# Performance work log

Hardware: AMD Instinct MI355X
Metric: run time of the kernel (lower is better)

Reference implementation:

```python
import jax, jax.numpy as jnp
import numpy as np

MARGIN = 0.5          # TripletLoss(margin=0.5)
N_FEAT = 100000       # gallery size N (rows of `features`)
D = 128               # embedding dim
N_BATCH = 256         # batch size n
N_CLASSES = 1000      # number of identities -> ~100 positives per class


def setup_inputs() -> dict:
    key = jax.random.key(0)
    k1, k2 = jax.random.split(key)
    inputs = jax.random.normal(k1, (N_BATCH, D), dtype=jnp.float32)
    features = jax.random.normal(k2, (N_FEAT, D), dtype=jnp.float32)
    # feature_labels encodes the t2i dict: label of every gallery row.
    feature_labels = (jnp.arange(N_FEAT, dtype=jnp.int32) % N_CLASSES).astype(jnp.int32)
    # idx[i] is the gallery row corresponding to batch sample i (distinct rows).
    idx = jnp.arange(N_BATCH, dtype=jnp.int32)
    # consistency: targets[i] must equal feature_labels[idx[i]]
    targets = feature_labels[idx]
    return {"inputs": inputs, "features": features, "targets": targets,
            "feature_labels": feature_labels, "idx": idx}


def reference(inputs, features, targets, feature_labels, idx):
    # sim_mat = inputs @ features.T  -> [n, N]
    sim = jnp.matmul(inputs, features.T)
    n_feat = features.shape[0]
    # pos: same identity, excluding the sample's own gallery row idx[i]
    same = feature_labels[None, :] == targets[:, None]          # [n, N]
    is_self = jnp.arange(n_feat, dtype=idx.dtype)[None, :] == idx[:, None]
    pos_mask = same & ~is_self
    neg_mask = ~same
    big = jnp.asarray(jnp.finfo(sim.dtype).max, sim.dtype)
    pos = jnp.min(jnp.where(pos_mask, sim, big), axis=1)        # hardest positive (min sim)
    neg = jnp.max(jnp.where(neg_mask, sim, -big), axis=1)       # hardest negative (max sim)
    loss = jax.nn.relu(neg - pos + MARGIN)                      # [n]
    return jnp.sum(loss) / targets.shape[0]
```

## Files before the change

### kernel.cpp

```cpp
#include <hip/hip_runtime.h>

#define NFEAT   100000
#define NBATCH  256
#define DIM     128
#define MARGIN_F 0.5f
#define FLT_BIG 3.402823466e+38f

#define GRID    250
#define CHUNKS  25
#define CROWS   16
#define RPB     (CHUNKS * CROWS)
#define CBYTES  (CROWS * DIM * 2)

#define GRIDF   1250
#define RPBF    80
#define NTILEF  5

typedef __bf16 bf8_t  __attribute__((ext_vector_type(8)));
typedef short  sh8_t  __attribute__((ext_vector_type(8)));
typedef float  f32x4  __attribute__((ext_vector_type(4)));

__device__ __forceinline__ bf8_t pack8(float4 v0, float4 v1) {
  bf8_t r;
  r[0] = (__bf16)v0.x; r[1] = (__bf16)v0.y; r[2] = (__bf16)v0.z; r[3] = (__bf16)v0.w;
  r[4] = (__bf16)v1.x; r[5] = (__bf16)v1.y; r[6] = (__bf16)v1.z; r[7] = (__bf16)v1.w;
  return r;
}

template <typename VA, typename VC>
__device__ __forceinline__ auto mfma_sel(VA a, VA b, VC c, int)
    -> decltype(__builtin_amdgcn_mfma_f32_16x16x32_bf16(a, b, c, 0, 0, 0)) {
  return __builtin_amdgcn_mfma_f32_16x16x32_bf16(a, b, c, 0, 0, 0);
}
template <typename VA, typename VC>
__device__ __forceinline__ VC mfma_sel(VA a, VA b, VC c, long) {
  return __builtin_amdgcn_mfma_f32_16x16x32_bf16(
      __builtin_bit_cast(sh8_t, a), __builtin_bit_cast(sh8_t, b), c, 0, 0, 0);
}
__device__ __forceinline__ f32x4 mfma_bf16(bf8_t a, bf8_t b, f32x4 c) {
  return mfma_sel(a, b, c, 0);
}

#if defined(__has_builtin)
#if __has_builtin(__builtin_amdgcn_global_load_lds)
#define HAVE_GLLDS 1
#endif
#endif

__device__ __forceinline__ void stage16(const char* g, char* l) {
#ifdef HAVE_GLLDS
  __builtin_amdgcn_global_load_lds(
      (const __attribute__((address_space(1))) unsigned int*)g,
      (__attribute__((address_space(3))) unsigned int*)l, 16, 0, 0);
#else
  *reinterpret_cast<float4*>(l) = *reinterpret_cast<const float4*>(g);
#endif
}

#define CFENCE()  asm volatile("" ::: "memory")
#define LGKM0()   asm volatile("s_waitcnt lgkmcnt(0)" ::: "memory")

#define NG_IN   (NBATCH * DIM / 8)
#define NG_ALL  (NG_IN + NFEAT * DIM / 8)
__global__ __launch_bounds__(256) void cast_bf16(
    const float* __restrict__ inputs, const float* __restrict__ features,
    __bf16* __restrict__ inb, __bf16* __restrict__ featb,
    float* __restrict__ out)
{
  if (blockIdx.x == 0 && threadIdx.x == 0) out[0] = 0.0f;
  const int gid    = blockIdx.x * 256 + threadIdx.x;
  const int stride = gridDim.x * 256;
  for (int i = gid; i < NG_ALL; i += stride) {
    const float* src; __bf16* dst;
    if (i < NG_IN) { src = inputs + (size_t)i * 8;           dst = inb   + (size_t)i * 8; }
    else           { src = features + (size_t)(i - NG_IN) * 8; dst = featb + (size_t)(i - NG_IN) * 8; }
    float4 v0 = *reinterpret_cast<const float4*>(src);
    float4 v1 = *reinterpret_cast<const float4*>(src + 4);
    *reinterpret_cast<bf8_t*>(dst) = pack8(v0, v1);
  }
}

__global__ __launch_bounds__(512, 2) void triplet_main(
    const __bf16* __restrict__ inb, const __bf16* __restrict__ featb,
    const int* __restrict__ targets, const int* __restrict__ flabels,
    const int* __restrict__ idx,
    float* __restrict__ ppos, float* __restrict__ pneg)
{
  __shared__ char sB[2][CBYTES];
  __shared__ int  slab[RPB];

  const int tid  = threadIdx.x;
  const int lane = tid & 63;
  const int wv   = tid >> 6;
  const int l15  = lane & 15;
  const int lg   = lane >> 4;
  const int m0   = wv * 32;
  const int blk  = blockIdx.x;
  const int rowbase = blk * RPB;

  bf8_t afrag[2][4];
#pragma unroll
  for (int mt = 0; mt < 2; ++mt)
#pragma unroll
    for (int ks = 0; ks < 4; ++ks)
      afrag[mt][ks] = *reinterpret_cast<const bf8_t*>(
          (const char*)inb + (size_t)(m0 + mt * 16 + l15) * 256 + ks * 64 + lg * 16);

  int meta[2][4];
#pragma unroll
  for (int mt = 0; mt < 2; ++mt)
#pragma unroll
    for (int rr = 0; rr < 4; ++rr) {
      const int row = m0 + mt * 16 + lg * 4 + rr;
      meta[mt][rr] = (idx[row] << 10) | targets[row];
    }
  int labv = 0;
  if (tid < RPB) labv = flabels[rowbase + tid];

  const char* gsrc = (const char*)featb + (size_t)rowbase * 256 + tid * 8;
  const int p    = tid * 8;
  const int prow = p >> 8;
  const int pd   = p ^ ((prow & 7) << 4);

  ushort4 rbuf[4];
  rbuf[0] = *reinterpret_cast<const ushort4*>(gsrc + 0 * CBYTES);
  rbuf[1] = *reinterpret_cast<const ushort4*>(gsrc + 1 * CBYTES);
  rbuf[2] = *reinterpret_cast<const ushort4*>(gsrc + 2 * CBYTES);
  rbuf[3] = *reinterpret_cast<const ushort4*>(gsrc + 3 * CBYTES);
  CFENCE();

  float minpos[2][4], maxneg[2][4];
#pragma unroll
  for (int mt = 0; mt < 2; ++mt)
#pragma unroll
    for (int rr = 0; rr < 4; ++rr) { minpos[mt][rr] = FLT_BIG; maxneg[mt][rr] = -FLT_BIG; }

  if (tid < RPB) slab[tid] = labv;
  *reinterpret_cast<ushort4*>(&sB[0][pd]) = rbuf[0];
  LGKM0();
  __builtin_amdgcn_s_barrier();
  CFENCE();

  const int swz = (l15 & 7) << 4;
#pragma unroll
  for (int c = 0; c < CHUNKS; ++c) {
    if (c + 4 < CHUNKS)
      rbuf[c & 3] = *reinterpret_cast<const ushort4*>(gsrc + (size_t)(c + 4) * CBYTES);

    const char* rb  = &sB[c & 1][l15 * 256];
    const int  j    = rowbase + c * CROWS + l15;
    const int  labj = slab[c * CROWS + l15];

    f32x4 acc0 = {0.f, 0.f, 0.f, 0.f};
    f32x4 acc1 = {0.f, 0.f, 0.f, 0.f};
#pragma unroll
    for (int ks = 0; ks < 4; ++ks) {
      bf8_t bf = *reinterpret_cast<const bf8_t*>(rb + ((ks * 64 + lg * 16) ^ swz));
      acc0 = mfma_bf16(afrag[0][ks], bf, acc0);
      acc1 = mfma_bf16(afrag[1][ks], bf, acc1);
    }
#pragma unroll
    for (int rr = 0; rr < 4; ++rr) {
      {
        const int  m    = meta[0][rr];
        const bool same = (labj == (m & 1023));
        const bool self = (j == (m >> 10));
        minpos[0][rr] = fminf(minpos[0][rr], (same && !self) ? acc0[rr] : FLT_BIG);
        maxneg[0][rr] = fmaxf(maxneg[0][rr], same ? -FLT_BIG : acc0[rr]);
      }
      {
        const int  m    = meta[1][rr];
        const bool same = (labj == (m & 1023));
        const bool self = (j == (m >> 10));
        minpos[1][rr] = fminf(minpos[1][rr], (same && !self) ? acc1[rr] : FLT_BIG);
        maxneg[1][rr] = fmaxf(maxneg[1][rr], same ? -FLT_BIG : acc1[rr]);
      }
    }

    if (c + 1 < CHUNKS)
      *reinterpret_cast<ushort4*>(&sB[(c + 1) & 1][pd]) = rbuf[(c + 1) & 3];

    LGKM0();
    __builtin_amdgcn_s_barrier();
    CFENCE();
  }

#pragma unroll
  for (int mt = 0; mt < 2; ++mt)
#pragma unroll
    for (int rr = 0; rr < 4; ++rr) {
      float mp = minpos[mt][rr], mn = maxneg[mt][rr];
#pragma unroll
      for (int m = 1; m < 16; m <<= 1) {
        mp = fminf(mp, __shfl_xor(mp, m, 64));
        mn = fmaxf(mn, __shfl_xor(mn, m, 64));
      }
      if (l15 == 0) {
        const int row = m0 + mt * 16 + lg * 4 + rr;
        ppos[blk * NBATCH + row] = mp;
        pneg[blk * NBATCH + row] = mn;
      }
    }
}

__global__ __launch_bounds__(512, 2) void triplet_partial_f32(
    const float* __restrict__ inputs, const float* __restrict__ features,
    const int* __restrict__ targets, const int* __restrict__ flabels,
    const int* __restrict__ idx,
    float* __restrict__ ppos, float* __restrict__ pneg,
    float* __restrict__ out)
{
  __shared__ char sB[RPBF * DIM * 4];

  const int tid  = threadIdx.x;
  const int lane = tid & 63;
  const int wv   = tid >> 6;
  const int l15  = lane & 15;
  const int lg   = lane >> 4;
  const int m0   = wv * 32;
  const int blk  = blockIdx.x;
  const int rowbase = blk * RPBF;

  if (blk == 0 && tid == 0) out[0] = 0.0f;

#pragma unroll
  for (int i = 0; i < NTILEF; ++i) {
    const int p    = i * 8192 + tid * 16;
    const int prow = p >> 9;
    const int scol = (p & 511) ^ ((prow & 7) << 4);
    stage16((const char*)features + (size_t)(rowbase + prow) * 512 + scol, &sB[p]);
  }

  bf8_t afrag[2][4];
#pragma unroll
  for (int mt = 0; mt < 2; ++mt) {
    const float* ap = inputs + (m0 + mt * 16 + l15) * DIM;
    float4 v0[4], v1[4];
#pragma unroll
    for (int ks = 0; ks < 4; ++ks) {
      const int k = ks * 32 + lg * 8;
      v0[ks] = *reinterpret_cast<const float4*>(ap + k);
      v1[ks] = *reinterpret_cast<const float4*>(ap + k + 4);
    }
#pragma unroll
    for (int ks = 0; ks < 4; ++ks)
      afrag[mt][ks] = pack8(v0[ks], v1[ks]);
  }

  int lab[NTILEF];
#pragma unroll
  for (int t = 0; t < NTILEF; ++t)
    lab[t] = flabels[rowbase + t * 16 + l15];

  int meta[2][4];
#pragma unroll
  for (int mt = 0; mt < 2; ++mt)
#pragma unroll
    for (int rr = 0; rr < 4; ++rr) {
      const int row = m0 + mt * 16 + lg * 4 + rr;
      meta[mt][rr] = (idx[row] << 10) | targets[row];
    }

  float minpos[2][4], maxneg[2][4];
#pragma unroll
  for (int mt = 0; mt < 2; ++mt)
#pragma unroll
    for (int rr = 0; rr < 4; ++rr) { minpos[mt][rr] = FLT_BIG; maxneg[mt][rr] = -FLT_BIG; }

  __syncthreads();

  const int swz = (l15 & 7) << 4;
#pragma unroll
  for (int t = 0; t < NTILEF; ++t) {
    const char* rbase = &sB[(t * 16 + l15) * 512];
    const int   j     = rowbase + t * 16 + l15;
    const int   labj  = lab[t];

    f32x4 acc0 = {0.f, 0.f, 0.f, 0.f};
    f32x4 acc1 = {0.f, 0.f, 0.f, 0.f};
#pragma unroll
    for (int ks = 0; ks < 4; ++ks) {
      const int o = ks * 128 + lg * 32;
      float4 v0 = *reinterpret_cast<const float4*>(rbase + ((o)      ^ swz));
      float4 v1 = *reinterpret_cast<const float4*>(rbase + ((o + 16) ^ swz));
      bf8_t bf = pack8(v0, v1);
      acc0 = mfma_bf16(afrag[0][ks], bf, acc0);
      acc1 = mfma_bf16(afrag[1][ks], bf, acc1);
    }
#pragma unroll
    for (int rr = 0; rr < 4; ++rr) {
      {
        const int  m = meta[0][rr];
        const bool same = (labj == (m & 1023));
        const bool self = (j == (m >> 10));
        minpos[0][rr] = fminf(minpos[0][rr], (same && !self) ? acc0[rr] : FLT_BIG);
        maxneg[0][rr] = fmaxf(maxneg[0][rr], same ? -FLT_BIG : acc0[rr]);
      }
      {
        const int  m = meta[1][rr];
        const bool same = (labj == (m & 1023));
        const bool self = (j == (m >> 10));
        minpos[1][rr] = fminf(minpos[1][rr], (same && !self) ? acc1[rr] : FLT_BIG);
        maxneg[1][rr] = fmaxf(maxneg[1][rr], same ? -FLT_BIG : acc1[rr]);
      }
    }
  }

#pragma unroll
  for (int mt = 0; mt < 2; ++mt)
#pragma unroll
    for (int rr = 0; rr < 4; ++rr) {
      float mp = minpos[mt][rr], mn = maxneg[mt][rr];
#pragma unroll
      for (int m = 1; m < 16; m <<= 1) {
        mp = fminf(mp, __shfl_xor(mp, m, 64));
        mn = fmaxf(mn, __shfl_xor(mn, m, 64));
      }
      if (l15 == 0) {
        const int row = m0 + mt * 16 + lg * 4 + rr;
        ppos[blk * NBATCH + row] = mp;
        pneg[blk * NBATCH + row] = mn;
      }
    }
}

__global__ __launch_bounds__(256) void triplet_reduce(
    const float* __restrict__ ppos, const float* __restrict__ pneg,
    float* __restrict__ out, int nblk)
{
  const int r = blockIdx.x;
  const int t = threadIdx.x;
  float mp = FLT_BIG, mn = -FLT_BIG;
  for (int b = t; b < nblk; b += 256) {
    mp = fminf(mp, ppos[b * NBATCH + r]);
    mn = fmaxf(mn, pneg[b * NBATCH + r]);
  }
#pragma unroll
  for (int m = 1; m < 64; m <<= 1) {
    mp = fminf(mp, __shfl_xor(mp, m, 64));
    mn = fmaxf(mn, __shfl_xor(mn, m, 64));
  }
  __shared__ float smp[4], smn[4];
  if ((t & 63) == 0) { smp[t >> 6] = mp; smn[t >> 6] = mn; }
  __syncthreads();
  if (t == 0) {
    mp = fminf(fminf(smp[0], smp[1]), fminf(smp[2], smp[3]));
    mn = fmaxf(fmaxf(smn[0], smn[1]), fmaxf(smn[2], smn[3]));
    float loss = mn - mp + MARGIN_F;
    loss = loss > 0.f ? loss : 0.f;
    atomicAdd(out, loss * (1.0f / NBATCH));
  }
}

extern "C" void kernel_launch(void* const* d_in, const int* in_sizes, int n_in,
                              void* d_out, int out_size, void* d_ws, size_t ws_size,
                              hipStream_t stream) {
  const float* inputs   = (const float*)d_in[0];
  const float* features = (const float*)d_in[1];
  const int*   targets  = (const int*)d_in[2];
  const int*   flabels  = (const int*)d_in[3];
  const int*   idx      = (const int*)d_in[4];
  float* out = (float*)d_out;

  const size_t featb_bytes = (size_t)NFEAT * DIM * 2;
  const size_t inb_bytes   = (size_t)NBATCH * DIM * 2;
  const size_t part_bytes  = (size_t)GRID * NBATCH * 4;

  if (ws_size >= featb_bytes + inb_bytes + 2 * part_bytes) {
    __bf16* featb = (__bf16*)d_ws;
    __bf16* inb   = (__bf16*)((char*)d_ws + featb_bytes);
    float*  ppos  = (float*)((char*)d_ws + featb_bytes + inb_bytes);
    float*  pneg  = ppos + (size_t)GRID * NBATCH;
    cast_bf16<<<2048, 256, 0, stream>>>(inputs, features, inb, featb, out);
    triplet_main<<<GRID, 512, 0, stream>>>(inb, featb, targets, flabels, idx, ppos, pneg);
    triplet_reduce<<<NBATCH, 256, 0, stream>>>(ppos, pneg, out, GRID);
  } else {
    float* ppos = (float*)d_ws;
    float* pneg = ppos + (size_t)GRIDF * NBATCH;
    triplet_partial_f32<<<GRIDF, 512, 0, stream>>>(inputs, features, targets,
                                                   flabels, idx, ppos, pneg, out);
    triplet_reduce<<<NBATCH, 256, 0, stream>>>(ppos, pneg, out, GRIDF);
  }
}
```

Before: 42.52 us.

## Load gallery tiles straight into registers and split batch across four blocks

```diff
diff --git a/kernel.cpp b/kernel.cpp
--- a/kernel.cpp
+++ b/kernel.cpp
@@ -6,11 +6,10 @@
 #define MARGIN_F 0.5f
 #define FLT_BIG 3.402823466e+38f
 
-#define GRID    250
-#define CHUNKS  25
-#define CROWS   16
-#define RPB     (CHUNKS * CROWS)
-#define CBYTES  (CROWS * DIM * 2)
+#define NCHUNK  625
+#define CROWS   160
+#define NTILE   10
+#define GRID    (NCHUNK * 4)
 
 #define GRIDF   1250
 #define RPBF    80
@@ -56,9 +55,6 @@
   *reinterpret_cast<float4*>(l) = *reinterpret_cast<const float4*>(g);
 #endif
 }
-
-#define CFENCE()  asm volatile("" ::: "memory")
-#define LGKM0()   asm volatile("s_waitcnt lgkmcnt(0)" ::: "memory")
 
 #define NG_IN   (NBATCH * DIM / 8)
 #define NG_ALL  (NG_IN + NFEAT * DIM / 8)
@@ -72,7 +68,7 @@
   const int stride = gridDim.x * 256;
   for (int i = gid; i < NG_ALL; i += stride) {
     const float* src; __bf16* dst;
-    if (i < NG_IN) { src = inputs + (size_t)i * 8;           dst = inb   + (size_t)i * 8; }
+    if (i < NG_IN) { src = inputs + (size_t)i * 8;             dst = inb   + (size_t)i * 8; }
     else           { src = features + (size_t)(i - NG_IN) * 8; dst = featb + (size_t)(i - NG_IN) * 8; }
     float4 v0 = *reinterpret_cast<const float4*>(src);
     float4 v1 = *reinterpret_cast<const float4*>(src + 4);
@@ -80,127 +76,111 @@
   }
 }
 
-__global__ __launch_bounds__(512, 2) void triplet_main(
+__global__ __launch_bounds__(256, 4) void triplet_main(
     const __bf16* __restrict__ inb, const __bf16* __restrict__ featb,
     const int* __restrict__ targets, const int* __restrict__ flabels,
     const int* __restrict__ idx,
     float* __restrict__ ppos, float* __restrict__ pneg)
 {
-  __shared__ char sB[2][CBYTES];
-  __shared__ int  slab[RPB];
-
-  const int tid  = threadIdx.x;
-  const int lane = tid & 63;
-  const int wv   = tid >> 6;
-  const int l15  = lane & 15;
-  const int lg   = lane >> 4;
-  const int m0   = wv * 32;
-  const int blk  = blockIdx.x;
-  const int rowbase = blk * RPB;
-
-  bf8_t afrag[2][4];
-#pragma unroll
-  for (int mt = 0; mt < 2; ++mt)
+  const int tid   = threadIdx.x;
+  const int lane  = tid & 63;
+  const int wv    = tid >> 6;
+  const int l15   = lane & 15;
+  const int lg    = lane >> 4;
+  const int blk   = blockIdx.x;
+  const int chunk = blk >> 2;
+  const int Mg    = blk & 3;
+  const int m0    = (Mg * 4 + wv) * 16;
+  const int frow0 = chunk * CROWS;
+
+  bf8_t afrag[4];
+  {
+    const char* abase = (const char*)inb + (size_t)(m0 + l15) * 256 + lg * 16;
 #pragma unroll
     for (int ks = 0; ks < 4; ++ks)
-      afrag[mt][ks] = *reinterpret_cast<const bf8_t*>(
-          (const char*)inb + (size_t)(m0 + mt * 16 + l15) * 256 + ks * 64 + lg * 16);
-
-  int meta[2][4];
-#pragma unroll
-  for (int mt = 0; mt < 2; ++mt)
-#pragma unroll
-    for (int rr = 0; rr < 4; ++rr) {
-      const int row = m0 + mt * 16 + lg * 4 + rr;
-      meta[mt][rr] = (idx[row] << 10) | targets[row];
-    }
-  int labv = 0;
-  if (tid < RPB) labv = flabels[rowbase + tid];
-
-  const char* gsrc = (const char*)featb + (size_t)rowbase * 256 + tid * 8;
-  const int p    = tid * 8;
-  const int prow = p >> 8;
-  const int pd   = p ^ ((prow & 7) << 4);
-
-  ushort4 rbuf[4];
-  rbuf[0] = *reinterpret_cast<const ushort4*>(gsrc + 0 * CBYTES);
-  rbuf[1] = *reinterpret_cast<const ushort4*>(gsrc + 1 * CBYTES);
-  rbuf[2] = *reinterpret_cast<const ushort4*>(gsrc + 2 * CBYTES);
-  rbuf[3] = *reinterpret_cast<const ushort4*>(gsrc + 3 * CBYTES);
-  CFENCE();
-
-  float minpos[2][4], maxneg[2][4];
-#pragma unroll
-  for (int mt = 0; mt < 2; ++mt)
-#pragma unroll
-    for (int rr = 0; rr < 4; ++rr) { minpos[mt][rr] = FLT_BIG; maxneg[mt][rr] = -FLT_BIG; }
-
-  if (tid < RPB) slab[tid] = labv;
-  *reinterpret_cast<ushort4*>(&sB[0][pd]) = rbuf[0];
-  LGKM0();
-  __builtin_amdgcn_s_barrier();
-  CFENCE();
-
-  const int swz = (l15 & 7) << 4;
-#pragma unroll
-  for (int c = 0; c < CHUNKS; ++c) {
-    if (c + 4 < CHUNKS)
-      rbuf[c & 3] = *reinterpret_cast<const ushort4*>(gsrc + (size_t)(c + 4) * CBYTES);
-
-    const char* rb  = &sB[c & 1][l15 * 256];
-    const int  j    = rowbase + c * CROWS + l15;
-    const int  labj = slab[c * CROWS + l15];
-
-    f32x4 acc0 = {0.f, 0.f, 0.f, 0.f};
-    f32x4 acc1 = {0.f, 0.f, 0.f, 0.f};
-#pragma unroll
-    for (int ks = 0; ks < 4; ++ks) {
-      bf8_t bf = *reinterpret_cast<const bf8_t*>(rb + ((ks * 64 + lg * 16) ^ swz));
-      acc0 = mfma_bf16(afrag[0][ks], bf, acc0);
-      acc1 = mfma_bf16(afrag[1][ks], bf, acc1);
-    }
-#pragma unroll
-    for (int rr = 0; rr < 4; ++rr) {
-      {
-        const int  m    = meta[0][rr];
-        const bool same = (labj == (m & 1023));
-        const bool self = (j == (m >> 10));
-        minpos[0][rr] = fminf(minpos[0][rr], (same && !self) ? acc0[rr] : FLT_BIG);
-        maxneg[0][rr] = fmaxf(maxneg[0][rr], same ? -FLT_BIG : acc0[rr]);
-      }
-      {
-        const int  m    = meta[1][rr];
-        const bool same = (labj == (m & 1023));
-        const bool self = (j == (m >> 10));
-        minpos[1][rr] = fminf(minpos[1][rr], (same && !self) ? acc1[rr] : FLT_BIG);
-        maxneg[1][rr] = fmaxf(maxneg[1][rr], same ? -FLT_BIG : acc1[rr]);
-      }
-    }
-
-    if (c + 1 < CHUNKS)
-      *reinterpret_cast<ushort4*>(&sB[(c + 1) & 1][pd]) = rbuf[(c + 1) & 3];
-
-    LGKM0();
-    __builtin_amdgcn_s_barrier();
-    CFENCE();
-  }
-
-#pragma unroll
-  for (int mt = 0; mt < 2; ++mt)
-#pragma unroll
-    for (int rr = 0; rr < 4; ++rr) {
-      float mp = minpos[mt][rr], mn = maxneg[mt][rr];
-#pragma unroll
-      for (int m = 1; m < 16; m <<= 1) {
-        mp = fminf(mp, __shfl_xor(mp, m, 64));
-        mn = fmaxf(mn, __shfl_xor(mn, m, 64));
-      }
-      if (l15 == 0) {
-        const int row = m0 + mt * 16 + lg * 4 + rr;
-        ppos[blk * NBATCH + row] = mp;
-        pneg[blk * NBATCH + row] = mn;
-      }
-    }
+      afrag[ks] = *reinterpret_cast<const bf8_t*>(abase + ks * 64);
+  }
+
+  int meta[4];
+#pragma unroll
+  for (int rr = 0; rr < 4; ++rr) {
+    const int row = m0 + lg * 4 + rr;
+    meta[rr] = (idx[row] << 10) | targets[row];
+  }
+
+  float minpos[4], maxneg[4];
+#pragma unroll
+  for (int rr = 0; rr < 4; ++rr) { minpos[rr] = FLT_BIG; maxneg[rr] = -FLT_BIG; }
+
+  const char* bbase = (const char*)featb + ((size_t)frow0 + l15) * 256 + lg * 16;
+  const int*  lbase = flabels + frow0 + l15;
+
+#define LOADB(buf, labv, t)                                        \
+  do {                                                             \
+    const char* p_ = bbase + (size_t)(t) * 4096;                   \
+    buf[0] = *reinterpret_cast<const bf8_t*>(p_);                  \
+    buf[1] = *reinterpret_cast<const bf8_t*>(p_ + 64);             \
+    buf[2] = *reinterpret_cast<const bf8_t*>(p_ + 128);            \
+    buf[3] = *reinterpret_cast<const bf8_t*>(p_ + 192);            \
+    labv = lbase[(t) * 16];                                        \
+  } while (0)
+
+#define EPILOGUE(acc, t, labj)                                     \
+  do {                                                             \
+    const int j_ = frow0 + (t) * 16 + l15;                         \
+    _Pragma("unroll")                                              \
+    for (int rr = 0; rr < 4; ++rr) {                               \
+      const int  m_   = meta[rr];                                  \
+      const bool same = ((labj) == (m_ & 1023));                   \
+      const bool self = (j_ == (m_ >> 10));                        \
+      minpos[rr] = fminf(minpos[rr], (same && !self) ? acc[rr] : FLT_BIG); \
+      maxneg[rr] = fmaxf(maxneg[rr], same ? -FLT_BIG : acc[rr]);   \
+    }                                                              \
+  } while (0)
+
+  bf8_t bA[4], bB[4];
+  int   labA, labB;
+  LOADB(bA, labA, 0);
+  LOADB(bB, labB, 1);
+
+#pragma unroll
+  for (int t = 0; t < NTILE; t += 2) {
+    {
+      f32x4 acc = {0.f, 0.f, 0.f, 0.f};
+#pragma unroll
+      for (int ks = 0; ks < 4; ++ks)
+        acc = mfma_bf16(afrag[ks], bA[ks], acc);
+      const int labj = labA;
+      if (t + 2 < NTILE) LOADB(bA, labA, t + 2);
+      EPILOGUE(acc, t, labj);
+    }
+    {
+      f32x4 acc = {0.f, 0.f, 0.f, 0.f};
+#pragma unroll
+      for (int ks = 0; ks < 4; ++ks)
+        acc = mfma_bf16(afrag[ks], bB[ks], acc);
+      const int labj = labB;
+      if (t + 3 < NTILE) LOADB(bB, labB, t + 3);
+      EPILOGUE(acc, t + 1, labj);
+    }
+  }
+#undef LOADB
+#undef EPILOGUE
+
+#pragma unroll
+  for (int rr = 0; rr < 4; ++rr) {
+    float mp = minpos[rr], mn = maxneg[rr];
+#pragma unroll
+    for (int m = 1; m < 16; m <<= 1) {
+      mp = fminf(mp, __shfl_xor(mp, m, 64));
+      mn = fmaxf(mn, __shfl_xor(mn, m, 64));
+    }
+    if (l15 == 0) {
+      const int row = m0 + lg * 4 + rr;
+      ppos[chunk * NBATCH + row] = mp;
+      pneg[chunk * NBATCH + row] = mn;
+    }
+  }
 }
 
 __global__ __launch_bounds__(512, 2) void triplet_partial_f32(
@@ -364,16 +344,16 @@
 
   const size_t featb_bytes = (size_t)NFEAT * DIM * 2;
   const size_t inb_bytes   = (size_t)NBATCH * DIM * 2;
-  const size_t part_bytes  = (size_t)GRID * NBATCH * 4;
+  const size_t part_bytes  = (size_t)NCHUNK * NBATCH * 4;
 
   if (ws_size >= featb_bytes + inb_bytes + 2 * part_bytes) {
     __bf16* featb = (__bf16*)d_ws;
     __bf16* inb   = (__bf16*)((char*)d_ws + featb_bytes);
     float*  ppos  = (float*)((char*)d_ws + featb_bytes + inb_bytes);
-    float*  pneg  = ppos + (size_t)GRID * NBATCH;
+    float*  pneg  = ppos + (size_t)NCHUNK * NBATCH;
     cast_bf16<<<2048, 256, 0, stream>>>(inputs, features, inb, featb, out);
-    triplet_main<<<GRID, 512, 0, stream>>>(inb, featb, targets, flabels, idx, ppos, pneg);
-    triplet_reduce<<<NBATCH, 256, 0, stream>>>(ppos, pneg, out, GRID);
+    triplet_main<<<GRID, 256, 0, stream>>>(inb, featb, targets, flabels, idx, ppos, pneg);
+    triplet_reduce<<<NBATCH, 256, 0, stream>>>(ppos, pneg, out, NCHUNK);
   } else {
     float* ppos = (float*)d_ws;
     float* pneg = ppos + (size_t)GRIDF * NBATCH;
```

After: 80.32 us. +88.9%, slower.
